# Kernel tuning notes

Hardware: AMD Instinct MI355X
Metric: run time of the kernel (lower is better)

The kernel has to match this reference:

```python
import jax, jax.numpy as jnp
import numpy as np

BS = 2
EMBED = 256
NH = 8
NL = 4
NP = 4
HD = EMBED // NH
SHAPES = [(128, 128), (64, 64), (32, 32), (16, 16)]
NQ = sum(h * w for h, w in SHAPES)  # 21760


def setup_inputs() -> dict:
    key = jax.random.key(0)
    ks = jax.random.split(key, 12)
    s = 1.0 / np.sqrt(EMBED)
    return {
        "query": jax.random.normal(ks[0], (BS, NQ, EMBED), jnp.float32),
        "reference_points": jax.random.uniform(ks[1], (BS, NQ, NL, 2), jnp.float32),
        "value": jax.random.normal(ks[2], (BS, NQ, EMBED), jnp.float32),
        "W_off": jax.random.normal(ks[3], (EMBED, NH * NL * NP * 2), jnp.float32) * 0.01,
        "b_off": jax.random.normal(ks[4], (NH * NL * NP * 2,), jnp.float32) * 0.5,
        "W_attn": jax.random.normal(ks[5], (EMBED, NH * NL * NP), jnp.float32) * 0.02,
        "b_attn": jnp.zeros((NH * NL * NP,), jnp.float32),
        "W_v": jax.random.normal(ks[6], (EMBED, EMBED), jnp.float32) * s,
        "b_v": jnp.zeros((EMBED,), jnp.float32),
        "W_out": jax.random.normal(ks[7], (EMBED, EMBED), jnp.float32) * s,
        "b_out": jnp.zeros((EMBED,), jnp.float32),
        "value_spatial_shapes": np.asarray(SHAPES, dtype=np.int64),
    }


def _ms_deform_attn(value, shapes, loc, aw):
    # value: [bs,V,nh,d]; loc: [bs,nq,nh,L,P,2] in [0,1]; aw: [bs,nq,nh,L,P]
    bs, V, nh, d = value.shape
    nq = loc.shape[1]
    out = jnp.zeros((bs, nq, nh, d), value.dtype)
    start = 0
    b_idx = jnp.arange(bs)[:, None, None, None]
    h_idx = jnp.arange(nh)[None, None, :, None]
    for l, (H, W) in enumerate(shapes):
        H, W = int(H), int(W)
        v = value[:, start:start + H * W].reshape(bs, H, W, nh, d)
        start += H * W
        g = 2.0 * loc[:, :, :, l] - 1.0  # [bs,nq,nh,P,2], grid_sample convention
        # align_corners=False pixel coordinates
        x = ((g[..., 0] + 1.0) * W - 1.0) * 0.5
        y = ((g[..., 1] + 1.0) * H - 1.0) * 0.5
        x0 = jnp.floor(x); y0 = jnp.floor(y)
        wx1 = x - x0; wx0 = 1.0 - wx1
        wy1 = y - y0; wy0 = 1.0 - wy1

        def gather(yi, xi):
            inb = (yi >= 0) & (yi < H) & (xi >= 0) & (xi < W)
            yc = jnp.clip(yi, 0, H - 1).astype(jnp.int32)
            xc = jnp.clip(xi, 0, W - 1).astype(jnp.int32)
            vals = v[b_idx, yc, xc, h_idx]  # [bs,nq,nh,P,d]
            return vals * inb[..., None].astype(v.dtype)

        samp = (gather(y0, x0) * (wy0 * wx0)[..., None]
                + gather(y0, x0 + 1) * (wy0 * wx1)[..., None]
                + gather(y0 + 1, x0) * (wy1 * wx0)[..., None]
                + gather(y0 + 1, x0 + 1) * (wy1 * wx1)[..., None])
        out = out + jnp.einsum('bqhpd,bqhp->bqhd', samp, aw[:, :, :, l])
    return out.reshape(bs, nq, nh * d)


def reference(query, reference_points, value, W_off, b_off, W_attn, b_attn,
              W_v, b_v, W_out, b_out, value_spatial_shapes):
    shapes = np.asarray(value_spatial_shapes)  # static [L,2]
    bs, nq, _ = query.shape
    v = (value @ W_v + b_v).reshape(bs, -1, NH, HD)
    off = (query @ W_off + b_off).reshape(bs, nq, NH, NL, NP, 2)
    aw = (query @ W_attn + b_attn).reshape(bs, nq, NH, NL * NP)
    aw = jax.nn.softmax(aw, axis=-1).reshape(bs, nq, NH, NL, NP)
    # offset normalizer: (W,H) per level
    norm = jnp.asarray(shapes[:, ::-1].astype(np.float32))  # [L,2]
    loc = reference_points[:, :, None, :, None, :] + off / norm[None, None, None, :, None, :]
    out = _ms_deform_attn(v, shapes, loc, aw)
    return out @ W_out + b_out
```

## Files before the change

kernel.cpp:

```cpp
#include <hip/hip_runtime.h>
#include <math.h>

#define BS 2
#define NQ 21760
#define V_LEN 21760
#define EMBED 256
#define NH 8
#define NL 4
#define NP 4
#define HD 32

typedef __bf16 bf16;
typedef __bf16 bf16x8 __attribute__((ext_vector_type(8)));
typedef __bf16 bf16x4 __attribute__((ext_vector_type(4)));
typedef float f32x4 __attribute__((ext_vector_type(4)));
typedef float f32x2 __attribute__((ext_vector_type(2)));
typedef unsigned int u32;

#define GLOAD_LDS16(gp, lp_) \
    __builtin_amdgcn_global_load_lds( \
        (const __attribute__((address_space(1))) unsigned int*)(gp), \
        (__attribute__((address_space(3))) unsigned int*)(lp_), 16, 0, 0)

__global__ __launch_bounds__(256) void cast_all(
    const float* __restrict__ W_v, const float* __restrict__ W_off,
    const float* __restrict__ W_attn, const float* __restrict__ W_out,
    const float* __restrict__ b_off, const float* __restrict__ b_attn,
    bf16* __restrict__ WTv, bf16* __restrict__ WToa, bf16* __restrict__ WTu,
    float* __restrict__ bcat)
{
    const int bid = blockIdx.x;
    const int tid = threadIdx.x;
    if (bid == 56) {
        if (tid < 384) bcat[tid] = (tid < 256) ? b_off[tid] : b_attn[tid - 256];
        return;
    }
    const float* W; bf16* WT; int N, tile;
    if (bid < 16)      { W = W_v;    WT = WTv;           N = 256; tile = bid; }
    else if (bid < 32) { W = W_off;  WT = WToa;          N = 256; tile = bid - 16; }
    else if (bid < 40) { W = W_attn; WT = WToa + 65536;  N = 128; tile = bid - 32; }
    else               { W = W_out;  WT = WTu;           N = 256; tile = bid - 40; }
    const int ntn = N >> 6;
    const int k0 = (tile / ntn) * 64, n0 = (tile % ntn) * 64;

    __shared__ float lds[64][65];
    const int c = tid & 63, r4 = tid >> 6;
    #pragma unroll
    for (int p = 0; p < 16; p++) {
        int rr = r4 + p * 4;
        lds[rr][c] = W[(size_t)(k0 + rr) * N + n0 + c];
    }
    __syncthreads();
    #pragma unroll
    for (int p = 0; p < 16; p++) {
        int i = r4 + p * 4;
        WT[(size_t)(n0 + i) * 256 + k0 + c] = (bf16)lds[c][i];
    }
}

template<bool A_F32, int OUT_MODE>
__global__ __launch_bounds__(256) void gemm_mfma(
    const void* __restrict__ Av, const bf16* __restrict__ WT,
    const float* __restrict__ bias, void* __restrict__ Cv,
    int N, int ntn)
{
    const int nmt = gridDim.x / ntn;
    const int bmt = blockIdx.x % nmt;
    const int bnt = blockIdx.x / nmt;
    const int bm = bmt * 128, bn = bnt * 128;

    __shared__ __align__(16) unsigned char AsRaw[2][A_F32 ? 128 * 32 * 4
                                                         : 128 * 32 * 2];

    const int tid = threadIdx.x;
    const int lane = tid & 63, wv = tid >> 6;
    const int wr = wv >> 1, wc = wv & 1;
    const int quad = lane >> 4, l16 = lane & 15;

    f32x4 acc[4][4];
    #pragma unroll
    for (int i = 0; i < 4; i++)
        #pragma unroll
        for (int j = 0; j < 4; j++)
            acc[i][j] = (f32x4){0.f, 0.f, 0.f, 0.f};

    const int b_row = tid >> 2, b_chunk = tid & 3;
    const int a_row8 = tid >> 3, a_phys = tid & 7;
    constexpr int NA = A_F32 ? 4 : 2;

    const bf16* bB[4];
    #pragma unroll
    for (int ni = 0; ni < 4; ni++)
        bB[ni] = WT + (size_t)(bn + wc * 64 + ni * 16 + l16) * 256 + quad * 8;

    auto stage = [&](int buf, int k0) {
        if constexpr (A_F32) {
            const float* A = (const float*)Av;
            #pragma unroll
            for (int p = 0; p < 4; p++) {
                int row = a_row8 + p * 32;
                int csrc = a_phys ^ (row & 7);
                GLOAD_LDS16(&A[(size_t)(bm + row) * 256 + k0 + csrc * 4],
                            &AsRaw[buf][p * 4096 + tid * 16]);
            }
        } else {
            const bf16* A = (const bf16*)Av;
            #pragma unroll
            for (int p = 0; p < 2; p++) {
                int row = b_row + p * 64;
                GLOAD_LDS16(&A[(size_t)(bm + row) * 256 + k0 + b_chunk * 8],
                            &AsRaw[buf][p * 4096 + tid * 16]);
            }
        }
    };

    stage(0, 0);
    int cur = 0;
    #pragma unroll
    for (int t = 0; t < 8; t++) {
        __builtin_amdgcn_s_barrier();
        bf16x8 bfr[4];
        #pragma unroll
        for (int ni = 0; ni < 4; ni++)
            bfr[ni] = *(const bf16x8*)(bB[ni] + t * 32);
        if (t < 7) {
            stage(cur ^ 1, (t + 1) * 32);
            asm volatile("s_waitcnt vmcnt(%0)" :: "n"(NA + 4) : "memory");
        } else {
            asm volatile("s_waitcnt vmcnt(4)" ::: "memory");
        }
        __builtin_amdgcn_s_barrier();

        bf16x8 af[4];
        if constexpr (A_F32) {
            const float* Asf = (const float*)&AsRaw[cur][0];
            #pragma unroll
            for (int mi = 0; mi < 4; mi++) {
                int r = wr * 64 + mi * 16 + l16;
                int g = r & 7;
                f32x4 u0 = *(const f32x4*)&Asf[r * 32 + ((2 * quad) ^ g) * 4];
                f32x4 u1 = *(const f32x4*)&Asf[r * 32 + ((2 * quad + 1) ^ g) * 4];
                bf16x8 hh;
                hh[0] = (bf16)u0[0]; hh[1] = (bf16)u0[1]; hh[2] = (bf16)u0[2]; hh[3] = (bf16)u0[3];
                hh[4] = (bf16)u1[0]; hh[5] = (bf16)u1[1]; hh[6] = (bf16)u1[2]; hh[7] = (bf16)u1[3];
                af[mi] = hh;
            }
        } else {
            const bf16* Asb = (const bf16*)&AsRaw[cur][0];
            #pragma unroll
            for (int mi = 0; mi < 4; mi++) {
                int r = wr * 64 + mi * 16 + l16;
                af[mi] = *(const bf16x8*)&Asb[r * 32 + quad * 8];
            }
        }
        #pragma unroll
        for (int mi = 0; mi < 4; mi++)
            #pragma unroll
            for (int ni = 0; ni < 4; ni++)
                acc[mi][ni] = __builtin_amdgcn_mfma_f32_16x16x32_bf16(
                    af[mi], bfr[ni], acc[mi][ni], 0, 0, 0);
        cur ^= 1;
    }

    #pragma unroll
    for (int mi = 0; mi < 4; mi++) {
        #pragma unroll
        for (int ni = 0; ni < 4; ni++) {
            const int col = bn + wc * 64 + ni * 16 + l16;
            const int row0 = bm + wr * 64 + mi * 16 + quad * 4;
            const float bc = bias[col];
            #pragma unroll
            for (int r = 0; r < 4; r++) {
                float v = acc[mi][ni][r] + bc;
                if constexpr (OUT_MODE == 0) {
                    ((float*)Cv)[(size_t)(row0 + r) * N + col] = v;
                } else if constexpr (OUT_MODE == 1) {
                    ((bf16*)Cv)[(size_t)(row0 + r) * N + col] = (bf16)v;
                } else {
                    int rv = row0 + r;
                    int bb = (rv >= V_LEN) ? 1 : 0;
                    int vv = rv - bb * V_LEN;
                    ((bf16*)Cv)[((size_t)(bb * NH + (col >> 5)) * V_LEN + vv) * 32
                                + (col & 31)] = (bf16)v;
                }
            }
        }
    }
}

__device__ inline void acc8(const uint4& rr, float ww,
                            f32x2& a01, f32x2& a23, f32x2& a45, f32x2& a67)
{
    f32x2 v;
    v[0] = __uint_as_float(rr.x << 16); v[1] = __uint_as_float(rr.x & 0xFFFF0000u); a01 += v * ww;
    v[0] = __uint_as_float(rr.y << 16); v[1] = __uint_as_float(rr.y & 0xFFFF0000u); a23 += v * ww;
    v[0] = __uint_as_float(rr.z << 16); v[1] = __uint_as_float(rr.z & 0xFFFF0000u); a45 += v * ww;
    v[0] = __uint_as_float(rr.w << 16); v[1] = __uint_as_float(rr.w & 0xFFFF0000u); a67 += v * ww;
}

__global__ __launch_bounds__(256) void deform_head(
    const bf16* __restrict__ vproj, const float* __restrict__ offaw,
    const float* __restrict__ refp, bf16* __restrict__ sampled)
{
    const int gid = blockIdx.x;
    const int idx8 = gid & 7;
    const int mid = gid >> 3;
    const int qg = mid % (NQ / 32);
    const int hsel = mid / (NQ / 32);
    const int h = (idx8 >> 1) + (hsel << 2);
    const int b = idx8 & 1;

    const int wv = threadIdx.x >> 6;
    const int t = threadIdx.x & 63;
    const int qq = t >> 3, e = t & 7;
    const int wq = wv * 8 + qq;
    const int q = qg * 32 + wq;
    const int bq = b * NQ + q;

    __shared__ int   s_idx[32][17];
    __shared__ __align__(16) float s_w[32][17][4];

    const float* row = offaw + (size_t)bq * 384;

    float l0 = row[256 + h * 16 + e];
    float l1 = row[256 + h * 16 + e + 8];
    float m = fmaxf(l0, l1);
    m = fmaxf(m, __shfl_xor(m, 1));
    m = fmaxf(m, __shfl_xor(m, 2));
    m = fmaxf(m, __shfl_xor(m, 4));
    float e0 = __expf(l0 - m), e1 = __expf(l1 - m);
    float ssum = e0 + e1;
    ssum += __shfl_xor(ssum, 1);
    ssum += __shfl_xor(ssum, 2);
    ssum += __shfl_xor(ssum, 4);
    float rs = 1.0f / ssum;
    float awv[2] = {e0 * rs, e1 * rs};

    #pragma unroll
    for (int sI = 0; sI < 2; sI++) {
        int lp = e + sI * 8;
        int l = lp >> 2;
        int Wl = 128 >> l, Hl = Wl;
        int st = (l == 0) ? 0 : (l == 1) ? 16384 : (l == 2) ? 20480 : 21504;
        float2 rp = *(const float2*)&refp[((size_t)bq * 4 + l) * 2];
        float2 oxy = *(const float2*)&row[h * 32 + lp * 2];
        float fW = (float)Wl, fH = (float)Hl;
        float x = (rp.x + oxy.x / fW) * fW - 0.5f;
        float y = (rp.y + oxy.y / fH) * fH - 0.5f;
        float xf = floorf(x), yf = floorf(y);
        int x0 = (int)xf, y0 = (int)yf;
        float wx1 = x - xf, wx0 = 1.f - wx1;
        float wy1 = y - yf, wy0 = 1.f - wy1;
        float aw = awv[sI];
        float wx0p = ((x0 >= 0) && (x0 < Wl)) ? wx0 : 0.f;
        float wx1p = ((x0 + 1 >= 0) && (x0 + 1 < Wl)) ? wx1 : 0.f;
        float wy0p = ((y0 >= 0) && (y0 < Hl)) ? wy0 : 0.f;
        float wy1p = ((y0 + 1 >= 0) && (y0 + 1 < Hl)) ? wy1 : 0.f;
        int px = min(max(x0, 0), Wl - 2), py = min(max(y0, 0), Hl - 2);
        int cx0 = min(max(x0, 0), Wl - 1), cx1 = min(max(x0 + 1, 0), Wl - 1);
        int cy0 = min(max(y0, 0), Hl - 1), cy1 = min(max(y0 + 1, 0), Hl - 1);
        float sx0 = ((cx0 == px) ? wx0p : 0.f) + ((cx1 == px) ? wx1p : 0.f);
        float sx1 = ((cx0 == px + 1) ? wx0p : 0.f) + ((cx1 == px + 1) ? wx1p : 0.f);
        float sy0 = ((cy0 == py) ? wy0p : 0.f) + ((cy1 == py) ? wy1p : 0.f);
        float sy1 = ((cy0 == py + 1) ? wy0p : 0.f) + ((cy1 == py + 1) ? wy1p : 0.f);
        s_idx[wq][lp] = (st + py * Wl + px) * 64;
        s_w[wq][lp][0] = sy0 * sx0 * aw;
        s_w[wq][lp][1] = sy1 * sx0 * aw;
        s_w[wq][lp][2] = sy0 * sx1 * aw;
        s_w[wq][lp][3] = sy1 * sx1 * aw;
    }

    const int j = t & 7;
    const int xslot = j >> 2, chgrp = j & 3;
    const char* vb = (const char*)vproj + (size_t)(b * NH + h) * V_LEN * 64;
    const int voffbase = j * 16;

    f32x2 a01 = {0.f, 0.f}, a23 = {0.f, 0.f}, a45 = {0.f, 0.f}, a67 = {0.f, 0.f};
    #pragma unroll
    for (int i = 0; i < 16; i++) {
        const int Wl = 128 >> (i >> 2);
        int off = s_idx[wq][i] + voffbase;
        f32x2 wp = *(const f32x2*)&s_w[wq][i][xslot * 2];
        uint4 r0 = *(const uint4*)(vb + off);
        uint4 r1 = *(const uint4*)(vb + off + Wl * 64);
        acc8(r0, wp[0], a01, a23, a45, a67);
        acc8(r1, wp[1], a01, a23, a45, a67);
    }

    float sarr[8] = {a01[0], a01[1], a23[0], a23[1], a45[0], a45[1], a67[0], a67[1]};
    #pragma unroll
    for (int i = 0; i < 8; i++) sarr[i] += __shfl_xor(sarr[i], 4);

    if ((t & 4) == 0) {
        bf16x8 o;
        #pragma unroll
        for (int i = 0; i < 8; i++) o[i] = (bf16)sarr[i];
        *(bf16x8*)&sampled[(size_t)bq * 256 + h * 32 + chgrp * 8] = o;
    }
}

extern "C" void kernel_launch(void* const* d_in, const int* in_sizes, int n_in,
                              void* d_out, int out_size, void* d_ws, size_t ws_size,
                              hipStream_t stream)
{
    const float* query  = (const float*)d_in[0];
    const float* refp   = (const float*)d_in[1];
    const float* value  = (const float*)d_in[2];
    const float* W_off  = (const float*)d_in[3];
    const float* b_off  = (const float*)d_in[4];
    const float* W_attn = (const float*)d_in[5];
    const float* b_attn = (const float*)d_in[6];
    const float* W_v    = (const float*)d_in[7];
    const float* b_v    = (const float*)d_in[8];
    const float* W_out  = (const float*)d_in[9];
    const float* b_out  = (const float*)d_in[10];
    float* out = (float*)d_out;

    const int M = BS * NQ;

    char* ws = (char*)d_ws;
    bf16*  WTv   = (bf16*)ws;                      ws += 256 * 256 * 2;
    bf16*  WToa  = (bf16*)ws;                      ws += 384 * 256 * 2;
    bf16*  WTu   = (bf16*)ws;                      ws += 256 * 256 * 2;
    float* bcat  = (float*)ws;                     ws += 384 * 4;
    bf16*  vproj = (bf16*)ws;                      ws += (size_t)M * 256 * 2;
    float* offaw = (float*)ws;                     ws += (size_t)M * 384 * 4;
    bf16*  samp  = (bf16*)ws;                      ws += (size_t)M * 256 * 2;

    cast_all<<<57, 256, 0, stream>>>(W_v, W_off, W_attn, W_out, b_off, b_attn,
                                     WTv, WToa, WTu, bcat);

    gemm_mfma<true, 2><<<(M / 128) * 2, 256, 0, stream>>>(value, WTv, b_v, vproj, 256, 2);
    gemm_mfma<true, 0><<<(M / 128) * 3, 256, 0, stream>>>(query, WToa, bcat, offaw, 384, 3);
    deform_head<<<2 * NH * (NQ / 32), 256, 0, stream>>>(vproj, offaw, refp, samp);
    gemm_mfma<false, 0><<<(M / 128) * 2, 256, 0, stream>>>(samp, WTu, b_out, out, 256, 2);
}
```

Measured before the change: 275.5 us.

## Stage GEMM weight tiles through LDS and software-pipeline deform sampling loads

The GEMM now double-buffers B (weight) tiles into shared memory with async global-to-LDS loads alongside A, replacing per-wave direct global reads of the weights. K becomes a runtime parameter and the k-loop is no longer unrolled. The deformable sampling kernel now precomputes offsets and issues gathers in groups of four points with two register buffers, so loads overlap the multiply-accumulate of the previous group. It also gains an occupancy hint of 4 blocks. The cost is extra LDS use and more registers per thread.

```diff
diff --git a/kernel.cpp b/kernel.cpp
--- a/kernel.cpp
+++ b/kernel.cpp
@@ -62,13 +62,14 @@
 __global__ __launch_bounds__(256) void gemm_mfma(
     const void* __restrict__ Av, const bf16* __restrict__ WT,
     const float* __restrict__ bias, void* __restrict__ Cv,
-    int N, int ntn)
+    int N, int K, int ntn)
 {
     const int nmt = gridDim.x / ntn;
     const int bmt = blockIdx.x % nmt;
     const int bnt = blockIdx.x / nmt;
     const int bm = bmt * 128, bn = bnt * 128;
 
+    __shared__ __align__(16) bf16 Bs[2][128 * 32];
     __shared__ __align__(16) unsigned char AsRaw[2][A_F32 ? 128 * 32 * 4
                                                          : 128 * 32 * 2];
 
@@ -86,12 +87,7 @@
 
     const int b_row = tid >> 2, b_chunk = tid & 3;
     const int a_row8 = tid >> 3, a_phys = tid & 7;
-    constexpr int NA = A_F32 ? 4 : 2;
-
-    const bf16* bB[4];
-    #pragma unroll
-    for (int ni = 0; ni < 4; ni++)
-        bB[ni] = WT + (size_t)(bn + wc * 64 + ni * 16 + l16) * 256 + quad * 8;
+    constexpr int NB = A_F32 ? 6 : 4;
 
     auto stage = [&](int buf, int k0) {
         if constexpr (A_F32) {
@@ -100,7 +96,7 @@
             for (int p = 0; p < 4; p++) {
                 int row = a_row8 + p * 32;
                 int csrc = a_phys ^ (row & 7);
-                GLOAD_LDS16(&A[(size_t)(bm + row) * 256 + k0 + csrc * 4],
+                GLOAD_LDS16(&A[(size_t)(bm + row) * K + k0 + csrc * 4],
                             &AsRaw[buf][p * 4096 + tid * 16]);
             }
         } else {
@@ -108,30 +104,32 @@
             #pragma unroll
             for (int p = 0; p < 2; p++) {
                 int row = b_row + p * 64;
-                GLOAD_LDS16(&A[(size_t)(bm + row) * 256 + k0 + b_chunk * 8],
+                GLOAD_LDS16(&A[(size_t)(bm + row) * K + k0 + b_chunk * 8],
                             &AsRaw[buf][p * 4096 + tid * 16]);
             }
         }
+        #pragma unroll
+        for (int p = 0; p < 2; p++) {
+            int row = b_row + p * 64;
+            GLOAD_LDS16(&WT[(size_t)(bn + row) * K + k0 + b_chunk * 8],
+                        (unsigned char*)&Bs[buf][0] + p * 4096 + tid * 16);
+        }
     };
 
+    const int nt = K >> 5;
     stage(0, 0);
     int cur = 0;
-    #pragma unroll
-    for (int t = 0; t < 8; t++) {
+    for (int t = 0; t < nt; t++) {
         __builtin_amdgcn_s_barrier();
-        bf16x8 bfr[4];
-        #pragma unroll
-        for (int ni = 0; ni < 4; ni++)
-            bfr[ni] = *(const bf16x8*)(bB[ni] + t * 32);
-        if (t < 7) {
-            stage(cur ^ 1, (t + 1) * 32);
-            asm volatile("s_waitcnt vmcnt(%0)" :: "n"(NA + 4) : "memory");
+        if (t + 1 < nt) {
+            stage(cur ^ 1, (t + 1) << 5);
+            asm volatile("s_waitcnt vmcnt(%0)" :: "n"(NB) : "memory");
         } else {
-            asm volatile("s_waitcnt vmcnt(4)" ::: "memory");
+            asm volatile("s_waitcnt vmcnt(0)" ::: "memory");
         }
         __builtin_amdgcn_s_barrier();
 
-        bf16x8 af[4];
+        bf16x8 af[4], bfr[4];
         if constexpr (A_F32) {
             const float* Asf = (const float*)&AsRaw[cur][0];
             #pragma unroll
@@ -152,6 +150,11 @@
                 int r = wr * 64 + mi * 16 + l16;
                 af[mi] = *(const bf16x8*)&Asb[r * 32 + quad * 8];
             }
+        }
+        #pragma unroll
+        for (int ni = 0; ni < 4; ni++) {
+            int r = wc * 64 + ni * 16 + l16;
+            bfr[ni] = *(const bf16x8*)&Bs[cur][r * 32 + quad * 8];
         }
         #pragma unroll
         for (int mi = 0; mi < 4; mi++)
@@ -198,7 +201,19 @@
     v[0] = __uint_as_float(rr.w << 16); v[1] = __uint_as_float(rr.w & 0xFFFF0000u); a67 += v * ww;
 }
 
-__global__ __launch_bounds__(256) void deform_head(
+template<int G>
+__device__ inline void load_group(const char* vb, const int* offv, uint4* r)
+{
+    #pragma unroll
+    for (int k = 0; k < 4; k++) {
+        const int i = G * 4 + k;
+        const int Wl = 128 >> (i >> 2);
+        r[k * 2 + 0] = *(const uint4*)(vb + offv[i]);
+        r[k * 2 + 1] = *(const uint4*)(vb + offv[i] + Wl * 64);
+    }
+}
+
+__global__ __launch_bounds__(256, 4) void deform_head(
     const bf16* __restrict__ vproj, const float* __restrict__ offaw,
     const float* __restrict__ refp, bf16* __restrict__ sampled)
 {
@@ -271,21 +286,36 @@
     }
 
     const int j = t & 7;
-    const int xslot = j >> 2, chgrp = j & 3;
+    const int xslot = j >> 2;
+    const int chgrp = j & 3;
     const char* vb = (const char*)vproj + (size_t)(b * NH + h) * V_LEN * 64;
     const int voffbase = j * 16;
 
+    int offv[16];
+    #pragma unroll
+    for (int i = 0; i < 16; i++) offv[i] = s_idx[wq][i] + voffbase;
+
     f32x2 a01 = {0.f, 0.f}, a23 = {0.f, 0.f}, a45 = {0.f, 0.f}, a67 = {0.f, 0.f};
-    #pragma unroll
-    for (int i = 0; i < 16; i++) {
-        const int Wl = 128 >> (i >> 2);
-        int off = s_idx[wq][i] + voffbase;
-        f32x2 wp = *(const f32x2*)&s_w[wq][i][xslot * 2];
-        uint4 r0 = *(const uint4*)(vb + off);
-        uint4 r1 = *(const uint4*)(vb + off + Wl * 64);
-        acc8(r0, wp[0], a01, a23, a45, a67);
-        acc8(r1, wp[1], a01, a23, a45, a67);
-    }
+
+    uint4 rA[8], rB[8];
+    auto mac_group = [&](const uint4* r, int G) {
+        #pragma unroll
+        for (int k = 0; k < 4; k++) {
+            const int i = G * 4 + k;
+            f32x2 wp = *(const f32x2*)&s_w[wq][i][xslot * 2];
+            acc8(r[k * 2 + 0], wp[0], a01, a23, a45, a67);
+            acc8(r[k * 2 + 1], wp[1], a01, a23, a45, a67);
+        }
+    };
+
+    load_group<0>(vb, offv, rA);
+    load_group<1>(vb, offv, rB);
+    mac_group(rA, 0);
+    load_group<2>(vb, offv, rA);
+    mac_group(rB, 1);
+    load_group<3>(vb, offv, rB);
+    mac_group(rA, 2);
+    mac_group(rB, 3);
 
     float sarr[8] = {a01[0], a01[1], a23[0], a23[1], a45[0], a45[1], a67[0], a67[1]};
     #pragma unroll
@@ -330,8 +360,8 @@
     cast_all<<<57, 256, 0, stream>>>(W_v, W_off, W_attn, W_out, b_off, b_attn,
                                      WTv, WToa, WTu, bcat);
 
-    gemm_mfma<true, 2><<<(M / 128) * 2, 256, 0, stream>>>(value, WTv, b_v, vproj, 256, 2);
-    gemm_mfma<true, 0><<<(M / 128) * 3, 256, 0, stream>>>(query, WToa, bcat, offaw, 384, 3);
+    gemm_mfma<true, 2><<<(M / 128) * 2, 256, 0, stream>>>(value, WTv, b_v, vproj, 256, 256, 2);
+    gemm_mfma<true, 0><<<(M / 128) * 3, 256, 0, stream>>>(query, WToa, bcat, offaw, 384, 256, 3);
     deform_head<<<2 * NH * (NQ / 32), 256, 0, stream>>>(vproj, offaw, refp, samp);
-    gemm_mfma<false, 0><<<(M / 128) * 2, 256, 0, stream>>>(samp, WTu, b_out, out, 256, 2);
-}
+    gemm_mfma<false, 0><<<(M / 128) * 2, 256, 0, stream>>>(samp, WTu, b_out, out, 256, 256, 2);
+}
```

Result: faster. 268.8 us (-2.4%).
